# Performance work log

Hardware: AMD Instinct MI355X
Metric: run time of the kernel (lower is better)

Reference implementation:

```python
import jax, jax.numpy as jnp
import numpy as np
import math

D_MODEL = 1024
LAYER_ID = 6
NUM_LAYERS = 12
B, T = 8, 2048
MIN_P = -1e38


def _init_params():
    C = D_MODEL
    r01 = LAYER_ID / (NUM_LAYERS - 1)
    r1a0 = 1.0 - LAYER_ID / NUM_LAYERS
    h = np.arange(C, dtype=np.float32)
    decay_speed = -5.0 + 8.0 * (h / (C - 1)) ** (0.7 + 1.3 * r01)
    zigzag = (((np.arange(C) + 1) % 3) - 1).astype(np.float32) * 0.5
    U = np.float32(math.log(0.3)) + zigzag
    xx = (np.arange(C, dtype=np.float32) / C).reshape(1, 1, C)
    tmk = xx ** r1a0
    tmv = xx ** r1a0 + 0.3 * r01
    tmr = xx ** (0.5 * r1a0)
    return (jnp.asarray(decay_speed), jnp.asarray(U), jnp.asarray(tmk, jnp.float32),
            jnp.asarray(tmv, jnp.float32), jnp.asarray(tmr, jnp.float32))


def setup_inputs() -> dict:
    key = jax.random.key(0)
    k0, k1, k2, k3, k4 = jax.random.split(key, 5)
    W, U, tmk, tmv, tmr = _init_params()
    C = D_MODEL
    s = 1.0 / math.sqrt(C)
    return {
        "x": jax.random.normal(k0, (B, T, C), jnp.float32),
        "W": W, "U": U,
        "time_mix_k": tmk, "time_mix_v": tmv, "time_mix_r": tmr,
        "Wk": jax.random.normal(k1, (C, C), jnp.float32) * s,
        "Wv": jax.random.normal(k2, (C, C), jnp.float32) * s,
        "Wr": jax.random.normal(k3, (C, C), jnp.float32) * s,
        "Wo": jax.random.normal(k4, (C, C), jnp.float32) * s,
    }


def _wkv(W, U, k, v):
    # W, U: [C]; k, v: [B, T, C]. Stable WKV recurrence with max-trick.
    w = -jnp.exp(W)  # negative decay, per channel
    Bb, Tt, Cc = k.shape
    aa0 = jnp.zeros((Bb, Cc), k.dtype)
    bb0 = jnp.zeros((Bb, Cc), k.dtype)
    pp0 = jnp.full((Bb, Cc), MIN_P, k.dtype)

    def step(carry, kv_t):
        aa, bb, pp = carry
        kt, vt = kv_t  # [B, C]
        ww = U + kt
        p = jnp.maximum(pp, ww)
        e1 = jnp.exp(pp - p)
        e2 = jnp.exp(ww - p)
        y = (e1 * aa + e2 * vt) / (e1 * bb + e2)
        ww2 = pp + w
        p2 = jnp.maximum(ww2, kt)
        e1b = jnp.exp(ww2 - p2)
        e2b = jnp.exp(kt - p2)
        return (e1b * aa + e2b * vt, e1b * bb + e2b, p2), y

    kT = jnp.swapaxes(k, 0, 1)  # [T, B, C]
    vT = jnp.swapaxes(v, 0, 1)
    _, yT = jax.lax.scan(step, (aa0, bb0, pp0), (kT, vT))
    return jnp.swapaxes(yT, 0, 1)  # [B, T, C]


def reference(x, W, U, time_mix_k, time_mix_v, time_mix_r, Wk, Wv, Wr, Wo):
    # token shift: prepend zero along T, drop last step
    xs = jnp.pad(x, ((0, 0), (1, 0), (0, 0)))[:, :-1]
    xk = x * time_mix_k + xs * (1.0 - time_mix_k)
    xv = x * time_mix_v + xs * (1.0 - time_mix_v)
    xr = x * time_mix_r + xs * (1.0 - time_mix_r)
    K = jnp.einsum('btc,dc->btd', xk, Wk)
    V = jnp.einsum('btc,dc->btd', xv, Wv)
    R = jnp.einsum('btc,dc->btd', xr, Wr)
    wkv = _wkv(W, U, K, V)
    hidden = jax.lax.stop_gradient(wkv[:, -1, :])
    rwkv = jax.nn.sigmoid(R) * wkv
    output = jnp.einsum('btc,dc->btd', rwkv, Wo)
    return output, hidden
```

## Files before the change

kernel.cpp:

```cpp
#include <hip/hip_runtime.h>

#define Bn 8
#define Tn 2048
#define Cn 1024
#define Mn (Bn * Tn)
#define LCH 64
#define NCH (Tn / LCH)

typedef __attribute__((ext_vector_type(8))) short short8;
typedef __attribute__((ext_vector_type(4))) float f32x4;

typedef const __attribute__((address_space(1))) void gas_void;
typedef __attribute__((address_space(3))) void las_void;

__device__ __forceinline__ unsigned short f2bf(float f) {
    unsigned int u = __float_as_uint(f);
    u += 0x7FFFu + ((u >> 16) & 1u);
    return (unsigned short)(u >> 16);
}
__device__ __forceinline__ float bf2f(unsigned short h) {
    return __uint_as_float(((unsigned int)h) << 16);
}

__global__ __launch_bounds__(256) void cvt_kernel(const float* __restrict__ src,
                                                  unsigned short* __restrict__ dst) {
    int i = blockIdx.x * 256 + threadIdx.x;
    float4 v = ((const float4*)src)[i];
    ushort4 o;
    o.x = f2bf(v.x); o.y = f2bf(v.y); o.z = f2bf(v.z); o.w = f2bf(v.w);
    ((ushort4*)dst)[i] = o;
}

__device__ __forceinline__ ushort4 mix4(const float4& a, const float4& s, const float4& m) {
    ushort4 o;
    o.x = f2bf(s.x + (a.x - s.x) * m.x);
    o.y = f2bf(s.y + (a.y - s.y) * m.y);
    o.z = f2bf(s.z + (a.z - s.z) * m.z);
    o.w = f2bf(s.w + (a.w - s.w) * m.w);
    return o;
}

__global__ __launch_bounds__(256) void mix_kernel(const float* __restrict__ x,
                                                  const float* __restrict__ tmk,
                                                  const float* __restrict__ tmv,
                                                  const float* __restrict__ tmr,
                                                  unsigned short* __restrict__ ak,
                                                  unsigned short* __restrict__ av,
                                                  unsigned short* __restrict__ ar) {
    int i = blockIdx.x * 256 + threadIdx.x;
    int c4 = i & 255;
    int t  = (i >> 8) & (Tn - 1);
    float4 xc = ((const float4*)x)[i];
    float4 xs = make_float4(0.f, 0.f, 0.f, 0.f);
    if (t > 0) xs = ((const float4*)x)[i - 256];
    float4 mk = ((const float4*)tmk)[c4];
    float4 mv = ((const float4*)tmv)[c4];
    float4 mr = ((const float4*)tmr)[c4];
    ((ushort4*)ak)[i] = mix4(xc, xs, mk);
    ((ushort4*)av)[i] = mix4(xc, xs, mv);
    ((ushort4*)ar)[i] = mix4(xc, xs, mr);
}


#define NT 16
#define BUFB 49152

#define PHASE_BAR() asm volatile("s_barrier" ::: "memory")
#define WAITV6()    asm volatile("s_waitcnt vmcnt(6)" ::: "memory")
#define WAITV0()    asm volatile("s_waitcnt vmcnt(0)" ::: "memory")

__device__ __forceinline__ void stage_rows(const unsigned short* gbase,
                                           char* ldsbase, int lane, int wid) {
    int rowg = wid * 16 + (lane >> 3);
    int slot = (lane & 7) ^ (lane >> 3);
    const unsigned short* s0 = gbase + (size_t)rowg * 1024 + slot * 8;
    const unsigned short* s1 = gbase + (size_t)(rowg + 8) * 1024 + slot * 8;
    char* d0 = ldsbase + (wid * 16) * 128;
    char* d1 = ldsbase + (wid * 16 + 8) * 128;
    __builtin_amdgcn_global_load_lds((gas_void*)s0, (las_void*)d0, 16, 0, 0);
    __builtin_amdgcn_global_load_lds((gas_void*)s1, (las_void*)d1, 16, 0, 0);
}

template <int FOUT>
__global__ __launch_bounds__(512, 2) void gemm_bt(const unsigned short* __restrict__ A,
                                                  const unsigned short* __restrict__ Bw,
                                                  unsigned short* __restrict__ Cb,
                                                  float* __restrict__ Cf) {
    __shared__ char lds[3 * BUFB];
    const int tid  = threadIdx.x;
    const int lane = tid & 63;
    const int wid  = tid >> 6;
    const int wr   = wid >> 2;
    const int wc   = wid & 3;
    const int bm   = blockIdx.x * 256;
    const int bn   = blockIdx.y * 128;

    const int lr = lane & 15;
    const int q  = lane >> 4;
    const int s7 = lr & 7;

    f32x4 acc[8][2] = {};

    stage_rows(A  + (size_t)bm * 1024,                 lds,                 lane, wid);
    stage_rows(A  + (size_t)(bm + 128) * 1024,         lds + 16384,         lane, wid);
    stage_rows(Bw + (size_t)bn * 1024,                 lds + 32768,         lane, wid);
    stage_rows(A  + (size_t)bm * 1024 + 64,            lds + BUFB,          lane, wid);
    stage_rows(A  + (size_t)(bm + 128) * 1024 + 64,    lds + BUFB + 16384,  lane, wid);
    stage_rows(Bw + (size_t)bn * 1024 + 64,            lds + BUFB + 32768,  lane, wid);
    WAITV6();
    PHASE_BAR();

    int cur = 0, nxt2 = 2;
#pragma unroll 1
    for (int t = 0; t < NT; ++t) {
        char* Ab = lds + cur * BUFB;
        char* Bb = Ab + 32768;
        const bool st = (t + 2) < NT;
        char* An = lds + nxt2 * BUFB;
        const unsigned short* gA = A  + (size_t)bm * 1024 + (t + 2) * 64;
        const unsigned short* gB = Bw + (size_t)bn * 1024 + (t + 2) * 64;

        short8 af[8], bf0, bf1;
        if (st) stage_rows(gA, An, lane, wid);
#pragma unroll
        for (int mi = 0; mi < 8; ++mi)
            af[mi] = *(const short8*)(Ab + (wr * 128 + mi * 16 + lr) * 128 + ((q ^ s7) << 4));
        bf0 = *(const short8*)(Bb + (wc * 32 + lr) * 128 + ((q ^ s7) << 4));
        __builtin_amdgcn_s_setprio(1);
#pragma unroll
        for (int mi = 0; mi < 8; ++mi)
            acc[mi][0] = __builtin_amdgcn_mfma_f32_16x16x32_bf16(af[mi], bf0, acc[mi][0], 0, 0, 0);
        __builtin_amdgcn_s_setprio(0);
        PHASE_BAR();

        if (st) stage_rows(gA + (size_t)128 * 1024, An + 16384, lane, wid);
        bf1 = *(const short8*)(Bb + (wc * 32 + 16 + lr) * 128 + ((q ^ s7) << 4));
        __builtin_amdgcn_s_setprio(1);
#pragma unroll
        for (int mi = 0; mi < 8; ++mi)
            acc[mi][1] = __builtin_amdgcn_mfma_f32_16x16x32_bf16(af[mi], bf1, acc[mi][1], 0, 0, 0);
        __builtin_amdgcn_s_setprio(0);
        PHASE_BAR();

        if (st) stage_rows(gB, An + 32768, lane, wid);
#pragma unroll
        for (int mi = 0; mi < 8; ++mi)
            af[mi] = *(const short8*)(Ab + (wr * 128 + mi * 16 + lr) * 128 + (((q | 4) ^ s7) << 4));
        bf0 = *(const short8*)(Bb + (wc * 32 + lr) * 128 + (((q | 4) ^ s7) << 4));
        __builtin_amdgcn_s_setprio(1);
#pragma unroll
        for (int mi = 0; mi < 8; ++mi)
            acc[mi][0] = __builtin_amdgcn_mfma_f32_16x16x32_bf16(af[mi], bf0, acc[mi][0], 0, 0, 0);
        __builtin_amdgcn_s_setprio(0);
        PHASE_BAR();

        bf1 = *(const short8*)(Bb + (wc * 32 + 16 + lr) * 128 + (((q | 4) ^ s7) << 4));
        __builtin_amdgcn_s_setprio(1);
#pragma unroll
        for (int mi = 0; mi < 8; ++mi)
            acc[mi][1] = __builtin_amdgcn_mfma_f32_16x16x32_bf16(af[mi], bf1, acc[mi][1], 0, 0, 0);
        __builtin_amdgcn_s_setprio(0);
        if (t <= NT - 3) { WAITV6(); } else { WAITV0(); }
        PHASE_BAR();

        cur  = (cur  == 2) ? 0 : cur + 1;
        nxt2 = (nxt2 == 2) ? 0 : nxt2 + 1;
    }

    const int crow0 = bm + wr * 128 + q * 4;
    const int ccol0 = bn + wc * 32 + lr;
#pragma unroll
    for (int mi = 0; mi < 8; ++mi) {
#pragma unroll
        for (int ni = 0; ni < 2; ++ni) {
            int col = ccol0 + ni * 16;
#pragma unroll
            for (int j = 0; j < 4; ++j) {
                size_t idx = (size_t)(crow0 + mi * 16 + j) * 1024 + col;
                float v = acc[mi][ni][j];
                if (FOUT) Cf[idx] = v;
                else      Cb[idx] = f2bf(v);
            }
        }
    }
}

__global__ __launch_bounds__(256) void wkv_pass1(const unsigned short* __restrict__ K,
                                                 const unsigned short* __restrict__ V,
                                                 const float* __restrict__ Wd,
                                                 float* __restrict__ caa,
                                                 float* __restrict__ cbb,
                                                 float* __restrict__ cpp) {
    int c = blockIdx.x * 256 + threadIdx.x;
    int j = blockIdx.y;
    int b = blockIdx.z;
    float w = -__expf(Wd[c]);
    float aa = 0.f, bb = 0.f, pp = -1e38f;
    size_t base = ((size_t)(b * Tn + j * LCH)) * Cn + c;
#pragma unroll 4
    for (int t = 0; t < LCH; ++t) {
        size_t idx = base + (size_t)t * Cn;
        float kt = bf2f(K[idx]);
        float vt = bf2f(V[idx]);
        float ww2 = pp + w;
        float p2  = fmaxf(ww2, kt);
        float e1  = __expf(ww2 - p2);
        float e2  = __expf(kt - p2);
        aa = e1 * aa + e2 * vt;
        bb = e1 * bb + e2;
        pp = p2;
    }
    size_t o = ((size_t)b * NCH + j) * Cn + c;
    caa[o] = aa; cbb[o] = bb; cpp[o] = pp;
}

__global__ __launch_bounds__(256) void wkv_pass2(const float* __restrict__ Wd,
                                                 const float* __restrict__ caa,
                                                 const float* __restrict__ cbb,
                                                 const float* __restrict__ cpp,
                                                 float* __restrict__ saa,
                                                 float* __restrict__ sbb,
                                                 float* __restrict__ spp) {
    int c = blockIdx.x * 256 + threadIdx.x;
    int b = blockIdx.y;
    float Lw = -__expf(Wd[c]) * (float)LCH;
    float aa = 0.f, bb = 0.f, pp = -1e38f;
    for (int j = 0; j < NCH; ++j) {
        size_t o = ((size_t)b * NCH + j) * Cn + c;
        saa[o] = aa; sbb[o] = bb; spp[o] = pp;
        float qa = caa[o], qb = cbb[o], qp = cpp[o];
        float ppd = pp + Lw;
        float p  = fmaxf(ppd, qp);
        float e1 = __expf(ppd - p);
        float e2 = __expf(qp - p);
        aa = e1 * aa + e2 * qa;
        bb = e1 * bb + e2 * qb;
        pp = p;
    }
}

__global__ __launch_bounds__(256) void wkv_pass3(const unsigned short* __restrict__ K,
                                                 const unsigned short* __restrict__ V,
                                                 const unsigned short* __restrict__ Rb,
                                                 const float* __restrict__ Wd,
                                                 const float* __restrict__ Ud,
                                                 const float* __restrict__ saa,
                                                 const float* __restrict__ sbb,
                                                 const float* __restrict__ spp,
                                                 unsigned short* __restrict__ rwkv,
                                                 float* __restrict__ hidden) {
    int c = blockIdx.x * 256 + threadIdx.x;
    int j = blockIdx.y;
    int b = blockIdx.z;
    float w = -__expf(Wd[c]);
    float u = Ud[c];
    size_t o = ((size_t)b * NCH + j) * Cn + c;
    float aa = saa[o], bb = sbb[o], pp = spp[o];
    size_t base = ((size_t)(b * Tn + j * LCH)) * Cn + c;
    float y = 0.f;
#pragma unroll 4
    for (int t = 0; t < LCH; ++t) {
        size_t idx = base + (size_t)t * Cn;
        float kt = bf2f(K[idx]);
        float vt = bf2f(V[idx]);
        float rt = bf2f(Rb[idx]);
        float ww = u + kt;
        float p  = fmaxf(pp, ww);
        float e1 = __expf(pp - p);
        float e2 = __expf(ww - p);
        y = __fdividef(e1 * aa + e2 * vt, e1 * bb + e2);
        float sr = __fdividef(1.f, 1.f + __expf(-rt));
        rwkv[idx] = f2bf(sr * y);
        float ww2 = pp + w;
        float p2  = fmaxf(ww2, kt);
        float e1b = __expf(ww2 - p2);
        float e2b = __expf(kt - p2);
        aa = e1b * aa + e2b * vt;
        bb = e1b * bb + e2b;
        pp = p2;
    }
    if (j == NCH - 1) hidden[b * Cn + c] = y;
}

extern "C" void kernel_launch(void* const* d_in, const int* in_sizes, int n_in,
                              void* d_out, int out_size, void* d_ws, size_t ws_size,
                              hipStream_t stream) {
    const float* x   = (const float*)d_in[0];
    const float* Wd  = (const float*)d_in[1];
    const float* Ud  = (const float*)d_in[2];
    const float* tmk = (const float*)d_in[3];
    const float* tmv = (const float*)d_in[4];
    const float* tmr = (const float*)d_in[5];
    const float* Wk  = (const float*)d_in[6];
    const float* Wv  = (const float*)d_in[7];
    const float* Wr  = (const float*)d_in[8];
    const float* Wo  = (const float*)d_in[9];

    float* out    = (float*)d_out;
    float* hidden = out + (size_t)Mn * Cn;

    const size_t MK = (size_t)Mn * Cn;
    const size_t CC = (size_t)Cn * Cn;
    unsigned short* ak  = (unsigned short*)d_ws;
    unsigned short* av  = ak + MK;
    unsigned short* ar  = av + MK;
    unsigned short* Kb  = ar + MK;
    unsigned short* Wkb = Kb + MK;
    unsigned short* Wvb = Wkb + CC;
    unsigned short* Wrb = Wvb + CC;
    unsigned short* Wob = Wrb + CC;
    unsigned short* Vb = ak;
    unsigned short* Rb = av;
    unsigned short* rw = ar;
    const size_t SB = (size_t)Bn * NCH * Cn;
    float* caa = (float*)Wkb;
    float* cbb = caa + SB;
    float* cpp = cbb + SB;
    float* saa = cpp + SB;
    float* sbb = saa + SB;
    float* spp = sbb + SB;

    cvt_kernel<<<dim3(CC / 1024), 256, 0, stream>>>(Wk, Wkb);
    cvt_kernel<<<dim3(CC / 1024), 256, 0, stream>>>(Wv, Wvb);
    cvt_kernel<<<dim3(CC / 1024), 256, 0, stream>>>(Wr, Wrb);
    cvt_kernel<<<dim3(CC / 1024), 256, 0, stream>>>(Wo, Wob);

    mix_kernel<<<dim3(MK / 1024), 256, 0, stream>>>(x, tmk, tmv, tmr, ak, av, ar);

    dim3 gg(Mn / 256, Cn / 128);
    gemm_bt<0><<<gg, 512, 0, stream>>>(ak, Wkb, Kb, nullptr);
    gemm_bt<0><<<gg, 512, 0, stream>>>(av, Wvb, Vb, nullptr);
    gemm_bt<0><<<gg, 512, 0, stream>>>(ar, Wrb, Rb, nullptr);

    dim3 gw(Cn / 256, NCH, Bn);
    wkv_pass1<<<gw, 256, 0, stream>>>(Kb, Vb, Wd, caa, cbb, cpp);
    wkv_pass2<<<dim3(Cn / 256, Bn), 256, 0, stream>>>(Wd, caa, cbb, cpp, saa, sbb, spp);
    wkv_pass3<<<gw, 256, 0, stream>>>(Kb, Vb, Rb, Wd, Ud, saa, sbb, spp, rw, hidden);

    gemm_bt<1><<<gg, 512, 0, stream>>>(rw, Wob, nullptr, out);
}
```

Before: 383.9 us.

## Enlarge GEMM tile to 256x256 with BK=32, 4-stage LDS ring and register prefetch

Restructures the bf16 GEMM from a 256x128 tile with BK=64 and a 3-buffer ring to a 256x256 tile with BK=32 and a 4-buffer ring. Fragments for the next k-step are loaded from LDS into registers while the current MFMAs run, using ping-pong register sets, and the XOR swizzle is changed to suit 64-byte rows. The aim is more MFMA work per loaded byte, halving the number of blocks, and overlapping LDS reads with compute. In exchange it doubles the accumulator registers (128 floats per thread) plus double fragment sets under launch_bounds(512,2), so spills or lower occupancy are a risk, and the grid drops to 256 blocks.

Result: faster. 362.3 us (-5.6%).

```diff
diff --git a/kernel.cpp b/kernel.cpp
--- a/kernel.cpp
+++ b/kernel.cpp
@@ -62,23 +62,90 @@
 }
 
 
-#define NT 16
-#define BUFB 49152
+#define BKg  32
+#define NTg  32
+#define ABYT (256 * BKg * 2)
+#define BUFBY (2 * ABYT)
 
 #define PHASE_BAR() asm volatile("s_barrier" ::: "memory")
-#define WAITV6()    asm volatile("s_waitcnt vmcnt(6)" ::: "memory")
+#define WAITV4()    asm volatile("s_waitcnt vmcnt(4)" ::: "memory")
 #define WAITV0()    asm volatile("s_waitcnt vmcnt(0)" ::: "memory")
 
-__device__ __forceinline__ void stage_rows(const unsigned short* gbase,
-                                           char* ldsbase, int lane, int wid) {
-    int rowg = wid * 16 + (lane >> 3);
-    int slot = (lane & 7) ^ (lane >> 3);
-    const unsigned short* s0 = gbase + (size_t)rowg * 1024 + slot * 8;
-    const unsigned short* s1 = gbase + (size_t)(rowg + 8) * 1024 + slot * 8;
-    char* d0 = ldsbase + (wid * 16) * 128;
-    char* d1 = ldsbase + (wid * 16 + 8) * 128;
-    __builtin_amdgcn_global_load_lds((gas_void*)s0, (las_void*)d0, 16, 0, 0);
-    __builtin_amdgcn_global_load_lds((gas_void*)s1, (las_void*)d1, 16, 0, 0);
+__device__ __forceinline__ void stage16(const unsigned short* gbase,
+                                        char* ldsdst, int lane) {
+    int r = lane >> 2;
+    int g = (lane & 3) ^ ((lane >> 3) & 3);
+    const unsigned short* src = gbase + (size_t)r * 1024 + g * 8;
+    __builtin_amdgcn_global_load_lds((gas_void*)src, (las_void*)ldsdst, 16, 0, 0);
+}
+
+__device__ __forceinline__ void gemm_body(int t,
+    const unsigned short* __restrict__ A, const unsigned short* __restrict__ Bw,
+    char* lds, int bm, int bn, int lane, int wid, int wr, int wc, int lr, int rsw,
+    short8* afc, short8* bfc, short8* afn, short8* bfn, f32x4 acc[8][4]) {
+    char* Ab = lds + (size_t)(t & 3) * BUFBY;
+    char* Bb = Ab + ABYT;
+    char* An = lds + (size_t)((t + 3) & 3) * BUFBY;
+    char* Bs = An + ABYT;
+    char* A1 = lds + (size_t)((t + 1) & 3) * BUFBY;
+    char* B1 = A1 + ABYT;
+    const bool st = (t + 3) < NTg;
+    const bool ra = (t + 1) < NTg;
+    const int k0 = (t + 3) * BKg;
+
+    if (st) stage16(A + (size_t)(bm + wid * 16) * 1024 + k0, An + wid * 16 * 64, lane);
+#pragma unroll
+    for (int mi = 4; mi < 8; ++mi)
+        afc[mi] = *(const short8*)(Ab + (wr * 128 + mi * 16 + lr) * 64 + rsw);
+    __builtin_amdgcn_s_setprio(1);
+#pragma unroll
+    for (int mi = 0; mi < 2; ++mi)
+#pragma unroll
+        for (int ni = 0; ni < 4; ++ni)
+            acc[mi][ni] = __builtin_amdgcn_mfma_f32_16x16x32_bf16(afc[mi], bfc[ni], acc[mi][ni], 0, 0, 0);
+    __builtin_amdgcn_s_setprio(0);
+    PHASE_BAR();
+
+    if (st) stage16(A + (size_t)(bm + 128 + wid * 16) * 1024 + k0, An + (128 + wid * 16) * 64, lane);
+    if (ra) {
+#pragma unroll
+        for (int ni = 0; ni < 4; ++ni)
+            bfn[ni] = *(const short8*)(B1 + (wc * 64 + ni * 16 + lr) * 64 + rsw);
+    }
+    __builtin_amdgcn_s_setprio(1);
+#pragma unroll
+    for (int mi = 2; mi < 4; ++mi)
+#pragma unroll
+        for (int ni = 0; ni < 4; ++ni)
+            acc[mi][ni] = __builtin_amdgcn_mfma_f32_16x16x32_bf16(afc[mi], bfc[ni], acc[mi][ni], 0, 0, 0);
+    __builtin_amdgcn_s_setprio(0);
+    PHASE_BAR();
+
+    if (st) stage16(Bw + (size_t)(bn + wid * 16) * 1024 + k0, Bs + wid * 16 * 64, lane);
+    if (ra) {
+#pragma unroll
+        for (int mi = 0; mi < 4; ++mi)
+            afn[mi] = *(const short8*)(A1 + (wr * 128 + mi * 16 + lr) * 64 + rsw);
+    }
+    __builtin_amdgcn_s_setprio(1);
+#pragma unroll
+    for (int mi = 4; mi < 6; ++mi)
+#pragma unroll
+        for (int ni = 0; ni < 4; ++ni)
+            acc[mi][ni] = __builtin_amdgcn_mfma_f32_16x16x32_bf16(afc[mi], bfc[ni], acc[mi][ni], 0, 0, 0);
+    __builtin_amdgcn_s_setprio(0);
+    PHASE_BAR();
+
+    if (st) stage16(Bw + (size_t)(bn + 128 + wid * 16) * 1024 + k0, Bs + (128 + wid * 16) * 64, lane);
+    __builtin_amdgcn_s_setprio(1);
+#pragma unroll
+    for (int mi = 6; mi < 8; ++mi)
+#pragma unroll
+        for (int ni = 0; ni < 4; ++ni)
+            acc[mi][ni] = __builtin_amdgcn_mfma_f32_16x16x32_bf16(afc[mi], bfc[ni], acc[mi][ni], 0, 0, 0);
+    __builtin_amdgcn_s_setprio(0);
+    if (st) { WAITV4(); } else { WAITV0(); }
+    PHASE_BAR();
 }
 
 template <int FOUT>
@@ -86,93 +153,52 @@
                                                   const unsigned short* __restrict__ Bw,
                                                   unsigned short* __restrict__ Cb,
                                                   float* __restrict__ Cf) {
-    __shared__ char lds[3 * BUFB];
+    __shared__ char lds[4 * BUFBY];
     const int tid  = threadIdx.x;
     const int lane = tid & 63;
     const int wid  = tid >> 6;
     const int wr   = wid >> 2;
     const int wc   = wid & 3;
     const int bm   = blockIdx.x * 256;
-    const int bn   = blockIdx.y * 128;
-
-    const int lr = lane & 15;
-    const int q  = lane >> 4;
-    const int s7 = lr & 7;
-
-    f32x4 acc[8][2] = {};
-
-    stage_rows(A  + (size_t)bm * 1024,                 lds,                 lane, wid);
-    stage_rows(A  + (size_t)(bm + 128) * 1024,         lds + 16384,         lane, wid);
-    stage_rows(Bw + (size_t)bn * 1024,                 lds + 32768,         lane, wid);
-    stage_rows(A  + (size_t)bm * 1024 + 64,            lds + BUFB,          lane, wid);
-    stage_rows(A  + (size_t)(bm + 128) * 1024 + 64,    lds + BUFB + 16384,  lane, wid);
-    stage_rows(Bw + (size_t)bn * 1024 + 64,            lds + BUFB + 32768,  lane, wid);
-    WAITV6();
-    PHASE_BAR();
-
-    int cur = 0, nxt2 = 2;
+    const int bn   = blockIdx.y * 256;
+
+    const int lr  = lane & 15;
+    const int rsw = (((lane >> 4) ^ ((lane >> 1) & 3)) << 4);
+
+    f32x4 acc[8][4] = {};
+    short8 afA[8], bfA[4], afB[8], bfB[4];
+
+#pragma unroll
+    for (int i = 0; i < 3; ++i) {
+        char* Ad = lds + (size_t)i * BUFBY;
+        int k0 = i * BKg;
+        stage16(A  + (size_t)(bm + wid * 16) * 1024 + k0,       Ad + wid * 16 * 64, lane);
+        stage16(A  + (size_t)(bm + 128 + wid * 16) * 1024 + k0, Ad + (128 + wid * 16) * 64, lane);
+        stage16(Bw + (size_t)(bn + wid * 16) * 1024 + k0,       Ad + ABYT + wid * 16 * 64, lane);
+        stage16(Bw + (size_t)(bn + 128 + wid * 16) * 1024 + k0, Ad + ABYT + (128 + wid * 16) * 64, lane);
+    }
+    WAITV4();
+    PHASE_BAR();
+
+#pragma unroll
+    for (int mi = 0; mi < 4; ++mi)
+        afA[mi] = *(const short8*)(lds + (wr * 128 + mi * 16 + lr) * 64 + rsw);
+#pragma unroll
+    for (int ni = 0; ni < 4; ++ni)
+        bfA[ni] = *(const short8*)(lds + ABYT + (wc * 64 + ni * 16 + lr) * 64 + rsw);
+
 #pragma unroll 1
-    for (int t = 0; t < NT; ++t) {
-        char* Ab = lds + cur * BUFB;
-        char* Bb = Ab + 32768;
-        const bool st = (t + 2) < NT;
-        char* An = lds + nxt2 * BUFB;
-        const unsigned short* gA = A  + (size_t)bm * 1024 + (t + 2) * 64;
-        const unsigned short* gB = Bw + (size_t)bn * 1024 + (t + 2) * 64;
-
-        short8 af[8], bf0, bf1;
-        if (st) stage_rows(gA, An, lane, wid);
-#pragma unroll
-        for (int mi = 0; mi < 8; ++mi)
-            af[mi] = *(const short8*)(Ab + (wr * 128 + mi * 16 + lr) * 128 + ((q ^ s7) << 4));
-        bf0 = *(const short8*)(Bb + (wc * 32 + lr) * 128 + ((q ^ s7) << 4));
-        __builtin_amdgcn_s_setprio(1);
-#pragma unroll
-        for (int mi = 0; mi < 8; ++mi)
-            acc[mi][0] = __builtin_amdgcn_mfma_f32_16x16x32_bf16(af[mi], bf0, acc[mi][0], 0, 0, 0);
-        __builtin_amdgcn_s_setprio(0);
-        PHASE_BAR();
-
-        if (st) stage_rows(gA + (size_t)128 * 1024, An + 16384, lane, wid);
-        bf1 = *(const short8*)(Bb + (wc * 32 + 16 + lr) * 128 + ((q ^ s7) << 4));
-        __builtin_amdgcn_s_setprio(1);
-#pragma unroll
-        for (int mi = 0; mi < 8; ++mi)
-            acc[mi][1] = __builtin_amdgcn_mfma_f32_16x16x32_bf16(af[mi], bf1, acc[mi][1], 0, 0, 0);
-        __builtin_amdgcn_s_setprio(0);
-        PHASE_BAR();
-
-        if (st) stage_rows(gB, An + 32768, lane, wid);
-#pragma unroll
-        for (int mi = 0; mi < 8; ++mi)
-            af[mi] = *(const short8*)(Ab + (wr * 128 + mi * 16 + lr) * 128 + (((q | 4) ^ s7) << 4));
-        bf0 = *(const short8*)(Bb + (wc * 32 + lr) * 128 + (((q | 4) ^ s7) << 4));
-        __builtin_amdgcn_s_setprio(1);
-#pragma unroll
-        for (int mi = 0; mi < 8; ++mi)
-            acc[mi][0] = __builtin_amdgcn_mfma_f32_16x16x32_bf16(af[mi], bf0, acc[mi][0], 0, 0, 0);
-        __builtin_amdgcn_s_setprio(0);
-        PHASE_BAR();
-
-        bf1 = *(const short8*)(Bb + (wc * 32 + 16 + lr) * 128 + (((q | 4) ^ s7) << 4));
-        __builtin_amdgcn_s_setprio(1);
-#pragma unroll
-        for (int mi = 0; mi < 8; ++mi)
-            acc[mi][1] = __builtin_amdgcn_mfma_f32_16x16x32_bf16(af[mi], bf1, acc[mi][1], 0, 0, 0);
-        __builtin_amdgcn_s_setprio(0);
-        if (t <= NT - 3) { WAITV6(); } else { WAITV0(); }
-        PHASE_BAR();
-
-        cur  = (cur  == 2) ? 0 : cur + 1;
-        nxt2 = (nxt2 == 2) ? 0 : nxt2 + 1;
-    }
-
-    const int crow0 = bm + wr * 128 + q * 4;
-    const int ccol0 = bn + wc * 32 + lr;
+    for (int t = 0; t < NTg; t += 2) {
+        gemm_body(t,     A, Bw, lds, bm, bn, lane, wid, wr, wc, lr, rsw, afA, bfA, afB, bfB, acc);
+        gemm_body(t + 1, A, Bw, lds, bm, bn, lane, wid, wr, wc, lr, rsw, afB, bfB, afA, bfA, acc);
+    }
+
+    const int crow0 = bm + wr * 128 + (lane >> 4) * 4;
+    const int ccol0 = bn + wc * 64 + lr;
 #pragma unroll
     for (int mi = 0; mi < 8; ++mi) {
 #pragma unroll
-        for (int ni = 0; ni < 2; ++ni) {
+        for (int ni = 0; ni < 4; ++ni) {
             int col = ccol0 + ni * 16;
 #pragma unroll
             for (int j = 0; j < 4; ++j) {
@@ -327,7 +353,7 @@
 
     mix_kernel<<<dim3(MK / 1024), 256, 0, stream>>>(x, tmk, tmv, tmr, ak, av, ar);
 
-    dim3 gg(Mn / 256, Cn / 128);
+    dim3 gg(Mn / 256, Cn / 256);
     gemm_bt<0><<<gg, 512, 0, stream>>>(ak, Wkb, Kb, nullptr);
     gemm_bt<0><<<gg, 512, 0, stream>>>(av, Wvb, Vb, nullptr);
     gemm_bt<0><<<gg, 512, 0, stream>>>(ar, Wrb, Rb, nullptr);
```
